# Optimization experiments

Measured on AMD Instinct MI355X. Metric: run time of the kernel, lower is better.

Reference implementation:

```python
import jax, jax.numpy as jnp
import numpy as np

SEMA_DIM = 1024
L1, L2, B = 256, 320, 64


def setup_inputs() -> dict:
    key = jax.random.key(0)
    k1, k2, kw1, kb1, kw2, kb2 = jax.random.split(key, 6)
    D = SEMA_DIM
    s = 1.0 / np.sqrt(D)
    return {
        "r1": jax.random.normal(k1, (L1, B, D), dtype=jnp.float32),
        "r2": jax.random.normal(k2, (L2, B, D), dtype=jnp.float32),
        "W1": jax.random.uniform(kw1, (D, D), jnp.float32, -s, s),
        "b1": jax.random.uniform(kb1, (D,), jnp.float32, -s, s),
        "W2": jax.random.uniform(kw2, (D, D), jnp.float32, -s, s),
        "b2": jax.random.uniform(kb2, (D,), jnp.float32, -s, s),
    }


def _mlp(x, W1, b1, W2, b2):
    # torch Linear: x @ W.T + b
    h = jax.nn.relu(x @ W1.T + b1)
    return h @ W2.T + b2


def reference(r1, r2, W1, b1, W2, b2):
    # (L, B, D) -> mlp -> (B, L, D)
    r1 = jnp.transpose(_mlp(r1, W1, b1, W2, b2), (1, 0, 2))  # [B, L1, D]
    r2 = jnp.transpose(_mlp(r2, W1, b1, W2, b2), (1, 0, 2))  # [B, L2, D]

    o = jnp.einsum("bid,bjd->bij", r1, r2)  # [B, L1, L2]
    o1 = jax.nn.softmax(o, axis=2)           # attend r1 -> r2
    o2 = jax.nn.softmax(o, axis=1)           # attend r2 -> r1

    r1_c = jnp.einsum("bij,bjd->bid", o1, r2)  # [B, L1, D]
    r2_c = jnp.einsum("bij,bid->bjd", o2, r1)  # [B, L2, D]

    r1_pool = jnp.concatenate([r1, r1_c], axis=-1).sum(axis=1) / r1.shape[1]  # [B, 2D]
    r2_pool = jnp.concatenate([r2, r2_c], axis=-1).sum(axis=1) / r2.shape[1]  # [B, 2D]
    return (r1_pool, r2_pool)
```

## Files before the change

kernel.cpp:

```cpp
#include <hip/hip_runtime.h>
#include <stdint.h>

#define L1C 256
#define L2C 320
#define BC  64
#define DC  1024

typedef __bf16 bf16_t;
typedef __bf16 bf16x8 __attribute__((ext_vector_type(8)));
typedef __bf16 bf16x4 __attribute__((ext_vector_type(4)));
typedef float  f32x4  __attribute__((ext_vector_type(4)));

__device__ __forceinline__ void gload16(const void* g, void* l) {
  __builtin_amdgcn_global_load_lds(
      (__attribute__((address_space(1))) void*)g,
      (__attribute__((address_space(3))) void*)l, 16, 0, 0);
}

__global__ __launch_bounds__(256)
void conv_kernel(const float* __restrict__ src, bf16_t* __restrict__ dst, int n4) {
  int i = blockIdx.x * 256 + threadIdx.x;
  const int stride = gridDim.x * 256;
  for (; i < n4; i += stride) {
    float4 v = ((const float4*)src)[i];
    bf16x4 o = { (__bf16)v.x, (__bf16)v.y, (__bf16)v.z, (__bf16)v.w };
    ((bf16x4*)dst)[i] = o;
  }
}

__global__ __launch_bounds__(256)
void w2t_kernel(const float* __restrict__ W2, bf16_t* __restrict__ W2T) {
  __shared__ float tile[32][33];
  const int tx = threadIdx.x & 31, ty = threadIdx.x >> 5;
  const int x0 = blockIdx.x * 32, y0 = blockIdx.y * 32;
#pragma unroll
  for (int k = 0; k < 32; k += 8)
    tile[ty + k][tx] = W2[(size_t)(y0 + ty + k) * 1024 + x0 + tx];
  __syncthreads();
#pragma unroll
  for (int k = 0; k < 32; k += 8)
    W2T[(size_t)(x0 + ty + k) * 1024 + y0 + tx] = (bf16_t)tile[tx][ty + k];
}

__global__ __launch_bounds__(256)
void wb_kernel(const float* __restrict__ W2, const float* __restrict__ b2,
               float* __restrict__ w2b) {
  const int dt = threadIdx.x & 15, kg = threadIdx.x >> 4;
  const int d = blockIdx.x * 16 + dt;
  float s = 0.f;
  for (int k = kg * 64; k < kg * 64 + 64; ++k)
    s += W2[(size_t)k * 1024 + d] * b2[k];
  __shared__ float red[16][17];
  red[kg][dt] = s;
  __syncthreads();
  if (kg == 0) {
    float t = 0.f;
#pragma unroll
    for (int g = 0; g < 16; ++g) t += red[g][dt];
    w2b[d] = t;
  }
}

__global__ __launch_bounds__(512, 2)
void mlp_gemm_f32a(const float* __restrict__ R1, const float* __restrict__ R2,
                   const bf16_t* __restrict__ W, const float* __restrict__ bias,
                   bf16_t* __restrict__ C, int Mtiles,
                   const float* __restrict__ w2b, float* __restrict__ tpart) {
  const int nwg = Mtiles * 4;
  const int cpx = nwg >> 3;
  const int wg  = ((int)blockIdx.x & 7) * cpx + ((int)blockIdx.x >> 3);
  const int mt = wg >> 2, nt = wg & 3;

  __shared__ __align__(16) char lds[147456];

  const int t    = threadIdx.x;
  const int lane = t & 63, wid = t >> 6;
  const int wm = wid >> 2, wn = wid & 3;
  const int rsel = lane & 15, hi = lane >> 4;
  const int t16 = t * 16;

  const int rT = t >> 3;
  const int gT = (t & 7) ^ (rT & 7);
  const float* Abase = (mt < 64) ? (R1 + (size_t)mt * 256 * 1024)
                                 : (R2 + (size_t)(mt - 64) * 256 * 1024);
  const float* pA[4];
#pragma unroll
  for (int l = 0; l < 4; ++l)
    pA[l] = Abase + (size_t)(l * 64 + rT) * 1024 + gT * 4;

  const int P0 = t16, P1 = 8192 + t16;
  const int Lg0 = P0 ^ ((P0 >> 3) & 0x30);
  const int Lg1 = P1 ^ ((P1 >> 3) & 0x30);
  const bf16_t* pB0 = W + (size_t)(nt * 256 + (Lg0 >> 6)) * 1024 + ((Lg0 & 63) >> 1);
  const bf16_t* pB1 = W + (size_t)(nt * 256 + (Lg1 >> 6)) * 1024 + ((Lg1 & 63) >> 1);

  const int rowA = wm * 128 + rsel;
  const int offA0 = (rowA << 7) + (((2 * hi)     ^ (rsel & 7)) << 4);
  const int offA1 = (rowA << 7) + (((2 * hi + 1) ^ (rsel & 7)) << 4);
  const int kchunk = (hi ^ ((rsel >> 1) & 3)) << 4;
  const int offB = 32768 + ((wn * 64 + rsel) << 6) + kchunk;

  f32x4 acc[8][4] = {};
  bf16x8 bfr[4];

#pragma unroll
  for (int p = 0; p < 2; ++p) {
    char* db = lds + p * 49152;
#pragma unroll
    for (int l = 0; l < 4; ++l) gload16(pA[l] + p * 32, db + l * 8192 + t16);
    gload16(pB0 + p * 32, db + 32768 + t16);
    gload16(pB1 + p * 32, db + 40960 + t16);
  }
  asm volatile("s_waitcnt vmcnt(6)" ::: "memory");
  __builtin_amdgcn_s_barrier();
  __builtin_amdgcn_sched_barrier(0);

  int cur = 0;
#pragma unroll 1
  for (int tt = 0; tt < 32; ++tt) {
    const char* rb = lds + cur * 49152;
    int nx = cur + 2; if (nx >= 3) nx -= 3;
    char* sb = lds + nx * 49152;
    const int ks = (tt + 2) * 32;
    bf16x8 af[4];
#pragma unroll
    for (int m = 0; m < 4; ++m) {
      f32x4 a0 = *(const f32x4*)(rb + offA0 + m * 2048);
      f32x4 a1 = *(const f32x4*)(rb + offA1 + m * 2048);
      af[m] = bf16x8{ (bf16_t)a0[0], (bf16_t)a0[1], (bf16_t)a0[2], (bf16_t)a0[3],
                      (bf16_t)a1[0], (bf16_t)a1[1], (bf16_t)a1[2], (bf16_t)a1[3] };
    }
#pragma unroll
    for (int n = 0; n < 4; ++n) bfr[n] = *(const bf16x8*)(rb + offB + n * 1024);
    if (tt < 30) {
#pragma unroll
      for (int l = 0; l < 4; ++l) gload16(pA[l] + ks, sb + l * 8192 + t16);
    }
    __builtin_amdgcn_s_setprio(1);
#pragma unroll
    for (int m = 0; m < 4; ++m)
#pragma unroll
      for (int n = 0; n < 4; ++n)
        acc[m][n] = __builtin_amdgcn_mfma_f32_16x16x32_bf16(af[m], bfr[n], acc[m][n], 0, 0, 0);
    __builtin_amdgcn_s_setprio(0);
    __builtin_amdgcn_s_barrier();
    __builtin_amdgcn_sched_barrier(0);
#pragma unroll
    for (int m = 0; m < 4; ++m) {
      f32x4 a0 = *(const f32x4*)(rb + offA0 + (m + 4) * 2048);
      f32x4 a1 = *(const f32x4*)(rb + offA1 + (m + 4) * 2048);
      af[m] = bf16x8{ (bf16_t)a0[0], (bf16_t)a0[1], (bf16_t)a0[2], (bf16_t)a0[3],
                      (bf16_t)a1[0], (bf16_t)a1[1], (bf16_t)a1[2], (bf16_t)a1[3] };
    }
    if (tt < 30) {
      gload16(pB0 + ks, sb + 32768 + t16);
      gload16(pB1 + ks, sb + 40960 + t16);
    }
    __builtin_amdgcn_s_setprio(1);
#pragma unroll
    for (int m = 0; m < 4; ++m)
#pragma unroll
      for (int n = 0; n < 4; ++n)
        acc[m + 4][n] = __builtin_amdgcn_mfma_f32_16x16x32_bf16(af[m], bfr[n], acc[m + 4][n], 0, 0, 0);
    __builtin_amdgcn_s_setprio(0);
    if (tt < 30)       asm volatile("s_waitcnt vmcnt(6)" ::: "memory");
    else if (tt == 30) asm volatile("s_waitcnt vmcnt(0)" ::: "memory");
    __builtin_amdgcn_s_barrier();
    __builtin_amdgcn_sched_barrier(0);
    cur = (cur + 1 == 3) ? 0 : cur + 1;
  }

  const int row0 = mt * 256 + wm * 128 + hi * 4;
  const int col0 = nt * 256 + wn * 64 + rsel;
  float bv[4];
#pragma unroll
  for (int n = 0; n < 4; ++n) bv[n] = bias[col0 + n * 16];
#pragma unroll
  for (int m = 0; m < 8; ++m) {
#pragma unroll
    for (int q = 0; q < 4; ++q) {
      const size_t rr = (size_t)(row0 + m * 16 + q) * 1024;
#pragma unroll
      for (int n = 0; n < 4; ++n) {
        float v = fmaxf(acc[m][n][q] + bv[n], 0.f);
        C[rr + col0 + n * 16] = (bf16_t)v;
      }
    }
  }

  {
    float wv[4];
#pragma unroll
    for (int n = 0; n < 4; ++n) wv[n] = w2b[col0 + n * 16];
    float* tp = tpart + (size_t)(nt * 4 + wn) * 36864;
#pragma unroll
    for (int m = 0; m < 8; ++m) {
#pragma unroll
      for (int q = 0; q < 4; ++q) {
        float s = 0.f;
#pragma unroll
        for (int n = 0; n < 4; ++n) {
          float v = fmaxf(acc[m][n][q] + bv[n], 0.f);
          v = (float)(bf16_t)v;
          s += v * wv[n];
        }
        s += __shfl_xor(s, 1);
        s += __shfl_xor(s, 2);
        s += __shfl_xor(s, 4);
        s += __shfl_xor(s, 8);
        if (rsel == 0)
          tp[row0 + m * 16 + q] = s;
      }
    }
  }
}

__global__ __launch_bounds__(256)
void t_red(const float* __restrict__ tp, float* __restrict__ tT1,
           float* __restrict__ tT2) {
  const int r = blockIdx.x * 256 + threadIdx.x;
  float s = 0.f;
#pragma unroll
  for (int k = 0; k < 16; ++k) s += tp[(size_t)k * 36864 + r];
  if (r < 16384) tT1[(r & 63) * L1C + (r >> 6)] = s;
  else {
    const int r2 = r - 16384;
    tT2[(r2 & 63) * L2C + (r2 >> 6)] = s;
  }
}

__global__ __launch_bounds__(512, 2)
void mlp_gemm8(const bf16_t* __restrict__ A, const bf16_t* __restrict__ W,
               const float* __restrict__ bias, bf16_t* __restrict__ C,
               int Mtiles, int relu) {
  const int nwg = Mtiles * 4;
  const int cpx = nwg >> 3;
  const int wg  = ((int)blockIdx.x & 7) * cpx + ((int)blockIdx.x >> 3);
  const int mt = wg >> 2, nt = wg & 3;

  __shared__ __align__(16) char lds[131072];

  const int t    = threadIdx.x;
  const int lane = t & 63, wid = t >> 6;
  const int wm = wid >> 2, wn = wid & 3;
  const int rsel = lane & 15, hi = lane >> 4;
  const int t16 = t * 16;

  const int P0 = t16, P1 = 8192 + t16;
  const int Lg0 = P0 ^ ((P0 >> 3) & 0x30);
  const int Lg1 = P1 ^ ((P1 >> 3) & 0x30);
  const int rS0 = Lg0 >> 6, cS0 = (Lg0 & 63) >> 1;
  const int rS1 = Lg1 >> 6, cS1 = (Lg1 & 63) >> 1;
  const bf16_t* pA0 = A + (size_t)(mt * 256 + rS0) * 1024 + cS0;
  const bf16_t* pA1 = A + (size_t)(mt * 256 + rS1) * 1024 + cS1;
  const bf16_t* pB0 = W + (size_t)(nt * 256 + rS0) * 1024 + cS0;
  const bf16_t* pB1 = W + (size_t)(nt * 256 + rS1) * 1024 + cS1;

  const int kchunk = (hi ^ ((rsel >> 1) & 3)) << 4;
  const int offA = ((wm * 128 + rsel) << 6) + kchunk;
  const int offB = 16384 + ((wn * 64 + rsel) << 6) + kchunk;

  f32x4 acc[8][4] = {};
  bf16x8 bfr[4];

#pragma unroll
  for (int p = 0; p < 3; ++p) {
    char* db = lds + p * 32768;
    gload16(pA0 + p * 32, db + t16);
    gload16(pA1 + p * 32, db + 8192 + t16);
    gload16(pB0 + p * 32, db + 16384 + t16);
    gload16(pB1 + p * 32, db + 24576 + t16);
  }
  asm volatile("s_waitcnt vmcnt(8)" ::: "memory");
  __builtin_amdgcn_s_barrier();
  __builtin_amdgcn_sched_barrier(0);

#pragma unroll 1
  for (int tt = 0; tt < 32; ++tt) {
    const char* rb = lds + (tt & 3) * 32768;
    char* sb = lds + ((tt + 3) & 3) * 32768;
    const int ks = (tt + 3) * 32;
    bf16x8 af[4];
#pragma unroll
    for (int m = 0; m < 4; ++m) af[m] = *(const bf16x8*)(rb + offA + m * 1024);
#pragma unroll
    for (int n = 0; n < 4; ++n) bfr[n] = *(const bf16x8*)(rb + offB + n * 1024);
    if (tt < 29) {
      gload16(pA0 + ks, sb + t16);
      gload16(pA1 + ks, sb + 8192 + t16);
    }
    __builtin_amdgcn_s_setprio(1);
#pragma unroll
    for (int m = 0; m < 4; ++m)
#pragma unroll
      for (int n = 0; n < 4; ++n)
        acc[m][n] = __builtin_amdgcn_mfma_f32_16x16x32_bf16(af[m], bfr[n], acc[m][n], 0, 0, 0);
    __builtin_amdgcn_s_setprio(0);
    __builtin_amdgcn_s_barrier();
    __builtin_amdgcn_sched_barrier(0);
#pragma unroll
    for (int m = 0; m < 4; ++m) af[m] = *(const bf16x8*)(rb + offA + (m + 4) * 1024);
    if (tt < 29) {
      gload16(pB0 + ks, sb + 16384 + t16);
      gload16(pB1 + ks, sb + 24576 + t16);
    }
    __builtin_amdgcn_s_setprio(1);
#pragma unroll
    for (int m = 0; m < 4; ++m)
#pragma unroll
      for (int n = 0; n < 4; ++n)
        acc[m + 4][n] = __builtin_amdgcn_mfma_f32_16x16x32_bf16(af[m], bfr[n], acc[m + 4][n], 0, 0, 0);
    __builtin_amdgcn_s_setprio(0);
    if (tt < 29)       asm volatile("s_waitcnt vmcnt(8)" ::: "memory");
    else if (tt == 29) asm volatile("s_waitcnt vmcnt(4)" ::: "memory");
    else if (tt == 30) asm volatile("s_waitcnt vmcnt(0)" ::: "memory");
    __builtin_amdgcn_s_barrier();
    __builtin_amdgcn_sched_barrier(0);
  }

  const int row0 = mt * 256 + wm * 128 + hi * 4;
  const int col0 = nt * 256 + wn * 64 + rsel;
  float bv[4];
#pragma unroll
  for (int n = 0; n < 4; ++n) bv[n] = bias[col0 + n * 16];
#pragma unroll
  for (int m = 0; m < 8; ++m) {
#pragma unroll
    for (int q = 0; q < 4; ++q) {
      const size_t rr = (size_t)(row0 + m * 16 + q) * 1024;
#pragma unroll
      for (int n = 0; n < 4; ++n) {
        float v = acc[m][n][q] + bv[n];
        if (relu) v = fmaxf(v, 0.f);
        C[rr + col0 + n * 16] = (bf16_t)v;
      }
    }
  }
}

__global__ __launch_bounds__(256)
void gemmK(const bf16_t* __restrict__ A, const bf16_t* __restrict__ W,
           float* __restrict__ P, int KS) {
  const int slice = (int)blockIdx.x >> 6;
  const int tl = (int)blockIdx.x & 63;
  const int mt = tl >> 3, nt = tl & 7;
  const int koff = slice * KS;

  const int f = threadIdx.x;
  const int lane = f & 63, w = f >> 6;
  const int sRow = f >> 2, sCol8 = (f & 3) * 8;

  const bf16_t* Ab = A + (size_t)mt * 128 * 1024 + (size_t)sRow * 1024 + sCol8;
  const bf16_t* Bb = W + (size_t)nt * 128 * 1024 + (size_t)sRow * 1024 + sCol8;

  __shared__ __align__(16) bf16_t sA[128 * 32];
  __shared__ __align__(16) bf16_t sB[128 * 32];
  bf16_t* sAp = sA + sRow * 32 + sCol8;
  bf16_t* sBp = sB + sRow * 32 + sCol8;

  const int wr = (w >> 1) * 64, wc = (w & 1) * 64;
  const int rsel = lane & 15, koff2 = (lane >> 4) * 8;
  const bf16_t* rA = sA + (wr + rsel) * 32 + koff2;
  const bf16_t* rB = sB + (wc + rsel) * 32 + koff2;

  f32x4 acc[4][4] = {};
  for (int kt = koff; kt < koff + KS; kt += 32) {
    __syncthreads();
    gload16(Ab + kt,             sAp);
    gload16(Ab + kt + 64 * 1024, sAp + 64 * 32);
    gload16(Bb + kt,             sBp);
    gload16(Bb + kt + 64 * 1024, sBp + 64 * 32);
    asm volatile("s_waitcnt vmcnt(0)" ::: "memory");
    __syncthreads();
    bf16x8 af[4], bfv[4];
#pragma unroll
    for (int m = 0; m < 4; ++m) af[m] = *(const bf16x8*)(rA + m * 16 * 32);
#pragma unroll
    for (int n = 0; n < 4; ++n) bfv[n] = *(const bf16x8*)(rB + n * 16 * 32);
#pragma unroll
    for (int m = 0; m < 4; ++m)
#pragma unroll
      for (int n = 0; n < 4; ++n)
        acc[m][n] = __builtin_amdgcn_mfma_f32_16x16x32_bf16(af[m], bfv[n], acc[m][n], 0, 0, 0);
  }

  float* Pb = P + (size_t)slice * 1048576;
  const int row0 = mt * 128 + wr + (lane >> 4) * 4;
  const int col0 = nt * 128 + wc + rsel;
#pragma unroll
  for (int n = 0; n < 4; ++n) {
    const int c = col0 + n * 16;
#pragma unroll
    for (int m = 0; m < 4; ++m) {
      const int r = row0 + m * 16;
#pragma unroll
      for (int q = 0; q < 4; ++q)
        Pb[(size_t)(r + q) * 1024 + c] = acc[m][n][q];
    }
  }
}

__global__ __launch_bounds__(256)
void g_reduce(const float* __restrict__ Gp, bf16_t* __restrict__ GB) {
  const int i4 = blockIdx.x * 256 + threadIdx.x;
  float4 a = ((const float4*)Gp)[i4];
  float4 b = ((const float4*)(Gp + 1048576))[i4];
  float4 c = ((const float4*)(Gp + 2097152))[i4];
  float4 d = ((const float4*)(Gp + 3145728))[i4];
  bf16x4 o = { (bf16_t)(a.x + b.x + c.x + d.x), (bf16_t)(a.y + b.y + c.y + d.y),
               (bf16_t)(a.z + b.z + c.z + d.z), (bf16_t)(a.w + b.w + c.w + d.w) };
  ((bf16x4*)GB)[i4] = o;
}

__global__ __launch_bounds__(256)
void pool_gemmK(const bf16_t* __restrict__ A, const bf16_t* __restrict__ W,
                float* __restrict__ P) {
  const int slice = (int)blockIdx.x >> 4;
  const int tl = (int)blockIdx.x & 15;
  const int mt = tl >> 3, nt = tl & 7;
  const int koff = slice * 128;

  const int f = threadIdx.x;
  const int lane = f & 63, w = f >> 6;
  const int sRow = f >> 2, sCol8 = (f & 3) * 8;

  const bf16_t* Ab = A + (size_t)mt * 128 * 1024 + (size_t)sRow * 1024 + sCol8;
  const bf16_t* Bb = W + (size_t)nt * 128 * 1024 + (size_t)sRow * 1024 + sCol8;

  __shared__ __align__(16) bf16_t sA[128 * 32];
  __shared__ __align__(16) bf16_t sB[128 * 32];
  bf16_t* sAp = sA + sRow * 32 + sCol8;
  bf16_t* sBp = sB + sRow * 32 + sCol8;

  const int wr = (w >> 1) * 64, wc = (w & 1) * 64;
  const int rsel = lane & 15, koff2 = (lane >> 4) * 8;
  const bf16_t* rA = sA + (wr + rsel) * 32 + koff2;
  const bf16_t* rB = sB + (wc + rsel) * 32 + koff2;

  f32x4 acc[4][4] = {};
  for (int kt = koff; kt < koff + 128; kt += 32) {
    __syncthreads();
    gload16(Ab + kt,             sAp);
    gload16(Ab + kt + 64 * 1024, sAp + 64 * 32);
    gload16(Bb + kt,             sBp);
    gload16(Bb + kt + 64 * 1024, sBp + 64 * 32);
    asm volatile("s_waitcnt vmcnt(0)" ::: "memory");
    __syncthreads();
    bf16x8 af[4], bfv[4];
#pragma unroll
    for (int m = 0; m < 4; ++m) af[m] = *(const bf16x8*)(rA + m * 16 * 32);
#pragma unroll
    for (int n = 0; n < 4; ++n) bfv[n] = *(const bf16x8*)(rB + n * 16 * 32);
#pragma unroll
    for (int m = 0; m < 4; ++m)
#pragma unroll
      for (int n = 0; n < 4; ++n)
        acc[m][n] = __builtin_amdgcn_mfma_f32_16x16x32_bf16(af[m], bfv[n], acc[m][n], 0, 0, 0);
  }

  float* Pb = P + (size_t)slice * 262144;
  const int row0 = mt * 128 + wr + (lane >> 4) * 4;
  const int col0 = nt * 128 + wc + rsel;
#pragma unroll
  for (int n = 0; n < 4; ++n) {
    const int c = col0 + n * 16;
#pragma unroll
    for (int m = 0; m < 4; ++m) {
      const int r = row0 + m * 16;
#pragma unroll
      for (int q = 0; q < 4; ++q)
        Pb[(size_t)(r + q) * 1024 + c] = acc[m][n][q];
    }
  }
}

__global__ __launch_bounds__(256)
void pool_reduce(const float* __restrict__ Pp, const float* __restrict__ b2,
                 float* __restrict__ out) {
  const int idx = blockIdx.x * 256 + threadIdx.x;
  const int r = idx >> 10, c = idx & 1023;
  float s = b2[c];
#pragma unroll
  for (int sl = 0; sl < 8; ++sl) s += Pp[(size_t)sl * 262144 + idx];
  const int g = r >> 6, b = r & 63;
  out[(size_t)(g >> 1) * 131072 + (size_t)b * 2048 + (g & 1) * 1024 + c] = s;
}

__global__ __launch_bounds__(256)
void logits_gemm(const bf16_t* __restrict__ Y1, const bf16_t* __restrict__ Y2,
                 float* __restrict__ O) {
  const int wg = ((int)blockIdx.x & 7) * 48 + ((int)blockIdx.x >> 3);
  const int b = wg / 6, t6 = wg % 6;
  const int mt = t6 / 3, nt = t6 % 3;

  __shared__ __align__(16) char lds[65536];

  const int t = threadIdx.x;
  const int lane = t & 63, w = t >> 6;
  const int sRow = t >> 2;
  const int sCol8 = (((t & 3) ^ ((t >> 3) & 3))) * 8;
  const int t16 = t * 16;

  const int i0 = mt * 128 + sRow;
  const int i1 = i0 + 64;
  int j0 = nt * 128 + sRow;      if (j0 > L2C - 1) j0 = L2C - 1;
  int j1 = nt * 128 + sRow + 64; if (j1 > L2C - 1) j1 = L2C - 1;
  const bf16_t* A0 = Y1 + ((size_t)i0 * BC + b) * DC + sCol8;
  const bf16_t* A1 = Y1 + ((size_t)i1 * BC + b) * DC + sCol8;
  const bf16_t* B0 = Y2 + ((size_t)j0 * BC + b) * DC + sCol8;
  const bf16_t* B1 = Y2 + ((size_t)j1 * BC + b) * DC + sCol8;

  const int wr = (w >> 1) * 64, wc = (w & 1) * 64;
  const int rsel = lane & 15, hi = lane >> 4;
  const int kchunk = (hi ^ ((rsel >> 1) & 3)) << 4;
  const int offA = ((wr + rsel) << 6) + kchunk;
  const int offB = 8192 + ((wc + rsel) << 6) + kchunk;

  f32x4 acc[4][4] = {};

#pragma unroll
  for (int p = 0; p < 3; ++p) {
    char* db = lds + p * 16384;
    gload16(A0 + p * 32, db + t16);
    gload16(A1 + p * 32, db + 4096 + t16);
    gload16(B0 + p * 32, db + 8192 + t16);
    gload16(B1 + p * 32, db + 12288 + t16);
  }
  asm volatile("s_waitcnt vmcnt(8)" ::: "memory");
  __builtin_amdgcn_s_barrier();
  __builtin_amdgcn_sched_barrier(0);

#pragma unroll 1
  for (int tt = 0; tt < 32; ++tt) {
    const char* rb = lds + (tt & 3) * 16384;
    char* sb = lds + ((tt + 3) & 3) * 16384;
    const int ks = (tt + 3) * 32;
    bf16x8 af[4], bfv[4];
#pragma unroll
    for (int m = 0; m < 4; ++m) af[m] = *(const bf16x8*)(rb + offA + m * 1024);
#pragma unroll
    for (int n = 0; n < 4; ++n) bfv[n] = *(const bf16x8*)(rb + offB + n * 1024);
    if (tt < 29) {
      gload16(A0 + ks, sb + t16);
      gload16(A1 + ks, sb + 4096 + t16);
      gload16(B0 + ks, sb + 8192 + t16);
      gload16(B1 + ks, sb + 12288 + t16);
    }
    __builtin_amdgcn_s_setprio(1);
#pragma unroll
    for (int m = 0; m < 4; ++m)
#pragma unroll
      for (int n = 0; n < 4; ++n)
        acc[m][n] = __builtin_amdgcn_mfma_f32_16x16x32_bf16(af[m], bfv[n], acc[m][n], 0, 0, 0);
    __builtin_amdgcn_s_setprio(0);
    if (tt < 29)       asm volatile("s_waitcnt vmcnt(8)" ::: "memory");
    else if (tt == 29) asm volatile("s_waitcnt vmcnt(4)" ::: "memory");
    else if (tt == 30) asm volatile("s_waitcnt vmcnt(0)" ::: "memory");
    __builtin_amdgcn_s_barrier();
    __builtin_amdgcn_sched_barrier(0);
  }

  float* Ob = O + (size_t)b * L1C * L2C;
  const int row0 = mt * 128 + wr + hi * 4;
  const int col0 = nt * 128 + wc + rsel;
#pragma unroll
  for (int n = 0; n < 4; ++n) {
    const int c = col0 + n * 16;
    if (c < L2C) {
#pragma unroll
      for (int m = 0; m < 4; ++m) {
        const int r = row0 + m * 16;
#pragma unroll
        for (int q = 0; q < 4; ++q)
          Ob[(size_t)(r + q) * L2C + c] = acc[m][n][q];
      }
    }
  }
}

__global__ __launch_bounds__(256)
void row_stats(const float* __restrict__ O, const float* __restrict__ tT2,
               float* __restrict__ rowM, float* __restrict__ rowInv) {
  const int gw = blockIdx.x * 4 + (threadIdx.x >> 6);
  const int lane = threadIdx.x & 63;
  const int b = gw >> 8;
  const float* row = O + (size_t)gw * L2C;
  const float* t2 = tT2 + b * L2C;
  float v[5];
  float m = -1e30f;
#pragma unroll
  for (int t = 0; t < 5; ++t) { v[t] = row[t * 64 + lane] + t2[t * 64 + lane]; m = fmaxf(m, v[t]); }
#pragma unroll
  for (int off = 32; off; off >>= 1) m = fmaxf(m, __shfl_xor(m, off));
  float s = 0.f;
#pragma unroll
  for (int t = 0; t < 5; ++t) s += __expf(v[t] - m);
#pragma unroll
  for (int off = 32; off; off >>= 1) s += __shfl_xor(s, off);
  if (lane == 0) { rowM[gw] = m; rowInv[gw] = 1.f / s; }
}

__global__ __launch_bounds__(256)
void col_stats_c1(const float* __restrict__ O, const float* __restrict__ tT1,
                  const float* __restrict__ tT2,
                  const float* __restrict__ rowM, const float* __restrict__ rowInv,
                  float* __restrict__ colM, float* __restrict__ colInv,
                  float* __restrict__ c1) {
  const int b = blockIdx.x / 5, jb = blockIdx.x % 5;
  const int jl = threadIdx.x & 63, ig = threadIdx.x >> 6;
  const int j = jb * 64 + jl;
  const float* Ob = O + (size_t)b * L1C * L2C + j;
  const float* rM = rowM + b * L1C;
  const float* rI = rowInv + b * L1C;
  const float* t1 = tT1 + b * L1C;
  const float t2j = tT2[b * L2C + j];
  float m = -1e30f, s = 0.f, cp = 0.f;
  for (int i = ig; i < L1C; i += 4) {
    float ov = Ob[(size_t)i * L2C];
    float v = ov + t1[i];
    float mn = fmaxf(m, v);
    s = s * __expf(m - mn) + __expf(v - mn);
    m = mn;
    cp += __expf(ov + t2j - rM[i]) * rI[i];
  }
  __shared__ float sm[4][64], ss[4][64], sc[4][64];
  sm[ig][jl] = m; ss[ig][jl] = s; sc[ig][jl] = cp;
  __syncthreads();
  if (ig == 0) {
    for (int g = 1; g < 4; ++g) {
      float mg = sm[g][jl], sg = ss[g][jl];
      float mn = fmaxf(m, mg);
      s = s * __expf(m - mn) + sg * __expf(mg - mn);
      m = mn;
      cp += sc[g][jl];
    }
    colM[b * L2C + j] = m;
    colInv[b * L2C + j] = 1.f / s;
    c1[b * L2C + j] = cp;
  }
}

__global__ __launch_bounds__(256)
void c2_kernel(const float* __restrict__ O, const float* __restrict__ tT1,
               const float* __restrict__ colM, const float* __restrict__ colInv,
               float* __restrict__ c2) {
  const int gw = blockIdx.x * 4 + (threadIdx.x >> 6);
  const int lane = threadIdx.x & 63;
  const int b = gw >> 8;
  const float* row = O + (size_t)gw * L2C;
  const float* cM = colM + b * L2C;
  const float* cI = colInv + b * L2C;
  const float t1i = tT1[b * L1C + (gw & 255)];
  float s = 0.f;
#pragma unroll
  for (int t = 0; t < 5; ++t) {
    const int j = t * 64 + lane;
    s += __expf(row[j] + t1i - cM[j]) * cI[j];
  }
#pragma unroll
  for (int off = 32; off; off >>= 1) s += __shfl_xor(s, off);
  if (lane == 0) c2[gw] = s;
}

__global__ __launch_bounds__(256)
void u_kernel(const bf16_t* __restrict__ H, const float* __restrict__ c1,
              const float* __restrict__ c2, bf16_t* __restrict__ Ub) {
  const int b = blockIdx.x >> 2;
  const int d = (blockIdx.x & 3) * 256 + threadIdx.x;
  const bf16_t* H2 = H + (size_t)L1C * BC * DC;
  float s1 = 0.f, s1c = 0.f, s2 = 0.f, s2c = 0.f;
  const float* c2b = c2 + b * L1C;
  for (int i = 0; i < L1C; ++i) {
    float v = (float)H[((size_t)i * BC + b) * DC + d];
    s1 += v; s1c += c2b[i] * v;
  }
  const float* c1b = c1 + b * L2C;
  for (int j = 0; j < L2C; ++j) {
    float v = (float)H2[((size_t)j * BC + b) * DC + d];
    s2 += v; s2c += c1b[j] * v;
  }
  Ub[(size_t)(0 * 64 + b) * 1024 + d] = (bf16_t)(s1  * (1.f / L1C));
  Ub[(size_t)(1 * 64 + b) * 1024 + d] = (bf16_t)(s2c * (1.f / L1C));
  Ub[(size_t)(2 * 64 + b) * 1024 + d] = (bf16_t)(s2  * (1.f / L2C));
  Ub[(size_t)(3 * 64 + b) * 1024 + d] = (bf16_t)(s1c * (1.f / L2C));
}

extern "C" void kernel_launch(void* const* d_in, const int* in_sizes, int n_in,
                              void* d_out, int out_size, void* d_ws, size_t ws_size,
                              hipStream_t stream) {
  const float* r1 = (const float*)d_in[0];
  const float* r2 = (const float*)d_in[1];
  const float* W1 = (const float*)d_in[2];
  const float* b1 = (const float*)d_in[3];
  const float* W2 = (const float*)d_in[4];
  const float* b2 = (const float*)d_in[5];
  float* out = (float*)d_out;
  char* ws = (char*)d_ws;

  const size_t M1 = (size_t)L1C * BC;
  const size_t M2 = (size_t)L2C * BC;
  const size_t Mt = M1 + M2;

  size_t off = 0;
  bf16_t* XB  = (bf16_t*)(ws + off); off += Mt * DC * 2;
  bf16_t* HB  = (bf16_t*)(ws + off); off += Mt * DC * 2;
  bf16_t* WB1 = (bf16_t*)(ws + off); off += (size_t)DC * DC * 2;
  bf16_t* WB2 = (bf16_t*)(ws + off); off += (size_t)DC * DC * 2;
  bf16_t* W2T = (bf16_t*)(ws + off); off += (size_t)DC * DC * 2;
  bf16_t* GB  = (bf16_t*)(ws + off); off += (size_t)DC * DC * 2;
  float* w2b   = (float*)(ws + off); off += 4096;
  float* zb    = (float*)(ws + off); off += 4096;
  float* tT1   = (float*)(ws + off); off += BC * L1C * 4;
  float* tT2   = (float*)(ws + off); off += BC * L2C * 4;
  float* rowM  = (float*)(ws + off); off += BC * L1C * 4;
  float* rowIv = (float*)(ws + off); off += BC * L1C * 4;
  float* colM  = (float*)(ws + off); off += BC * L2C * 4;
  float* colIv = (float*)(ws + off); off += BC * L2C * 4;
  float* c1v   = (float*)(ws + off); off += BC * L2C * 4;
  float* c2v   = (float*)(ws + off); off += BC * L1C * 4;
  bf16_t* Ub   = (bf16_t*)(ws + off); off += 256 * DC * 2;
  float* tpart = (float*)(ws + off); off += (size_t)16 * Mt * 4;

  bf16_t* Z = XB;
  float*  O = (float*)((char*)XB + 35651584);
  float*  Gpart = (float*)((char*)XB + 58720256);
  float*  Ppart = (float*)HB;
  bf16_t* H2 = HB + M1 * DC;

  conv_kernel<<<512, 256, 0, stream>>>(W1, WB1, (int)((size_t)DC * DC / 4));
  conv_kernel<<<512, 256, 0, stream>>>(W2, WB2, (int)((size_t)DC * DC / 4));
  w2t_kernel<<<dim3(32, 32), 256, 0, stream>>>(W2, W2T);
  wb_kernel<<<64, 256, 0, stream>>>(W2, b2, w2b);
  (void)hipMemsetAsync(zb, 0, 4096, stream);

  mlp_gemm_f32a<<<576, 512, 0, stream>>>(r1, r2, WB1, b1, HB, 144, w2b, tpart);
  t_red<<<144, 256, 0, stream>>>(tpart, tT1, tT2);

  gemmK<<<256, 256, 0, stream>>>(W2T, W2T, Gpart, 256);
  g_reduce<<<1024, 256, 0, stream>>>(Gpart, GB);

  mlp_gemm8<<<256, 512, 0, stream>>>(HB, GB, zb, Z, 64, 0);

  logits_gemm<<<384, 256, 0, stream>>>(Z, H2, O);

  row_stats<<<4096, 256, 0, stream>>>(O, tT2, rowM, rowIv);
  col_stats_c1<<<320, 256, 0, stream>>>(O, tT1, tT2, rowM, rowIv, colM, colIv, c1v);
  c2_kernel<<<4096, 256, 0, stream>>>(O, tT1, colM, colIv, c2v);

  u_kernel<<<256, 256, 0, stream>>>(HB, c1v, c2v, Ub);
  pool_gemmK<<<128, 256, 0, stream>>>(Ub, WB2, Ppart);
  pool_reduce<<<1024, 256, 0, stream>>>(Ppart, b2, out);
}
```

Baseline: 304.0 us.

## Pre-convert activations to bf16 and use 128x128 first-layer GEMM with separate t reduction

Replaces the fused first-layer GEMM, which loaded fp32 activations into LDS and converted them per tile, with two steps. A separate conversion pass now writes bf16 copies of r1/r2, and a smaller 128x128-tile, 256-thread GEMM runs with a 4-stage LDS pipeline. The fused t-vector epilogue is replaced by a standalone kernel that re-reads H and dots each row with w2b. This trades extra global traffic (conversion pass, re-reading H) for higher occupancy, cheaper LDS fragment loads and no in-loop conversion.

```diff
diff --git a/kernel.cpp b/kernel.cpp
--- a/kernel.cpp
+++ b/kernel.cpp
@@ -61,122 +61,82 @@
   }
 }
 
-__global__ __launch_bounds__(512, 2)
-void mlp_gemm_f32a(const float* __restrict__ R1, const float* __restrict__ R2,
-                   const bf16_t* __restrict__ W, const float* __restrict__ bias,
-                   bf16_t* __restrict__ C, int Mtiles,
-                   const float* __restrict__ w2b, float* __restrict__ tpart) {
-  const int nwg = Mtiles * 4;
-  const int cpx = nwg >> 3;
-  const int wg  = ((int)blockIdx.x & 7) * cpx + ((int)blockIdx.x >> 3);
-  const int mt = wg >> 2, nt = wg & 3;
-
-  __shared__ __align__(16) char lds[147456];
-
-  const int t    = threadIdx.x;
-  const int lane = t & 63, wid = t >> 6;
-  const int wm = wid >> 2, wn = wid & 3;
+__global__ __launch_bounds__(256)
+void gemm1_128(const bf16_t* __restrict__ A, const bf16_t* __restrict__ W,
+               const float* __restrict__ bias, bf16_t* __restrict__ C) {
+  const int wg = ((int)blockIdx.x & 7) * 288 + ((int)blockIdx.x >> 3);
+  const int mt = wg >> 3, nt = wg & 7;
+
+  __shared__ __align__(16) char lds[65536];
+
+  const int t = threadIdx.x;
+  const int lane = t & 63, w = t >> 6;
+  const int sRow = t >> 2;
+  const int sCol8 = (((t & 3) ^ ((t >> 3) & 3))) * 8;
+  const int t16 = t * 16;
+
+  const bf16_t* A0 = A + (size_t)(mt * 128 + sRow) * 1024 + sCol8;
+  const bf16_t* A1 = A0 + (size_t)64 * 1024;
+  const bf16_t* B0 = W + (size_t)(nt * 128 + sRow) * 1024 + sCol8;
+  const bf16_t* B1 = B0 + (size_t)64 * 1024;
+
+  const int wr = (w >> 1) * 64, wc = (w & 1) * 64;
   const int rsel = lane & 15, hi = lane >> 4;
-  const int t16 = t * 16;
-
-  const int rT = t >> 3;
-  const int gT = (t & 7) ^ (rT & 7);
-  const float* Abase = (mt < 64) ? (R1 + (size_t)mt * 256 * 1024)
-                                 : (R2 + (size_t)(mt - 64) * 256 * 1024);
-  const float* pA[4];
-#pragma unroll
-  for (int l = 0; l < 4; ++l)
-    pA[l] = Abase + (size_t)(l * 64 + rT) * 1024 + gT * 4;
-
-  const int P0 = t16, P1 = 8192 + t16;
-  const int Lg0 = P0 ^ ((P0 >> 3) & 0x30);
-  const int Lg1 = P1 ^ ((P1 >> 3) & 0x30);
-  const bf16_t* pB0 = W + (size_t)(nt * 256 + (Lg0 >> 6)) * 1024 + ((Lg0 & 63) >> 1);
-  const bf16_t* pB1 = W + (size_t)(nt * 256 + (Lg1 >> 6)) * 1024 + ((Lg1 & 63) >> 1);
-
-  const int rowA = wm * 128 + rsel;
-  const int offA0 = (rowA << 7) + (((2 * hi)     ^ (rsel & 7)) << 4);
-  const int offA1 = (rowA << 7) + (((2 * hi + 1) ^ (rsel & 7)) << 4);
   const int kchunk = (hi ^ ((rsel >> 1) & 3)) << 4;
-  const int offB = 32768 + ((wn * 64 + rsel) << 6) + kchunk;
-
-  f32x4 acc[8][4] = {};
-  bf16x8 bfr[4];
-
-#pragma unroll
-  for (int p = 0; p < 2; ++p) {
-    char* db = lds + p * 49152;
-#pragma unroll
-    for (int l = 0; l < 4; ++l) gload16(pA[l] + p * 32, db + l * 8192 + t16);
-    gload16(pB0 + p * 32, db + 32768 + t16);
-    gload16(pB1 + p * 32, db + 40960 + t16);
-  }
-  asm volatile("s_waitcnt vmcnt(6)" ::: "memory");
+  const int offA = ((wr + rsel) << 6) + kchunk;
+  const int offB = 8192 + ((wc + rsel) << 6) + kchunk;
+
+  f32x4 acc[4][4] = {};
+
+#pragma unroll
+  for (int p = 0; p < 3; ++p) {
+    char* db = lds + p * 16384;
+    gload16(A0 + p * 32, db + t16);
+    gload16(A1 + p * 32, db + 4096 + t16);
+    gload16(B0 + p * 32, db + 8192 + t16);
+    gload16(B1 + p * 32, db + 12288 + t16);
+  }
+  asm volatile("s_waitcnt vmcnt(8)" ::: "memory");
   __builtin_amdgcn_s_barrier();
   __builtin_amdgcn_sched_barrier(0);
 
-  int cur = 0;
 #pragma unroll 1
   for (int tt = 0; tt < 32; ++tt) {
-    const char* rb = lds + cur * 49152;
-    int nx = cur + 2; if (nx >= 3) nx -= 3;
-    char* sb = lds + nx * 49152;
-    const int ks = (tt + 2) * 32;
-    bf16x8 af[4];
-#pragma unroll
-    for (int m = 0; m < 4; ++m) {
-      f32x4 a0 = *(const f32x4*)(rb + offA0 + m * 2048);
-      f32x4 a1 = *(const f32x4*)(rb + offA1 + m * 2048);
-      af[m] = bf16x8{ (bf16_t)a0[0], (bf16_t)a0[1], (bf16_t)a0[2], (bf16_t)a0[3],
-                      (bf16_t)a1[0], (bf16_t)a1[1], (bf16_t)a1[2], (bf16_t)a1[3] };
-    }
-#pragma unroll
-    for (int n = 0; n < 4; ++n) bfr[n] = *(const bf16x8*)(rb + offB + n * 1024);
-    if (tt < 30) {
-#pragma unroll
-      for (int l = 0; l < 4; ++l) gload16(pA[l] + ks, sb + l * 8192 + t16);
+    const char* rb = lds + (tt & 3) * 16384;
+    char* sb = lds + ((tt + 3) & 3) * 16384;
+    const int ks = (tt + 3) * 32;
+    bf16x8 af[4], bfv[4];
+#pragma unroll
+    for (int m = 0; m < 4; ++m) af[m] = *(const bf16x8*)(rb + offA + m * 1024);
+#pragma unroll
+    for (int n = 0; n < 4; ++n) bfv[n] = *(const bf16x8*)(rb + offB + n * 1024);
+    if (tt < 29) {
+      gload16(A0 + ks, sb + t16);
+      gload16(A1 + ks, sb + 4096 + t16);
+      gload16(B0 + ks, sb + 8192 + t16);
+      gload16(B1 + ks, sb + 12288 + t16);
     }
     __builtin_amdgcn_s_setprio(1);
 #pragma unroll
     for (int m = 0; m < 4; ++m)
 #pragma unroll
       for (int n = 0; n < 4; ++n)
-        acc[m][n] = __builtin_amdgcn_mfma_f32_16x16x32_bf16(af[m], bfr[n], acc[m][n], 0, 0, 0);
+        acc[m][n] = __builtin_amdgcn_mfma_f32_16x16x32_bf16(af[m], bfv[n], acc[m][n], 0, 0, 0);
     __builtin_amdgcn_s_setprio(0);
-    __builtin_amdgcn_s_barrier();
-    __builtin_amdgcn_sched_barrier(0);
-#pragma unroll
-    for (int m = 0; m < 4; ++m) {
-      f32x4 a0 = *(const f32x4*)(rb + offA0 + (m + 4) * 2048);
-      f32x4 a1 = *(const f32x4*)(rb + offA1 + (m + 4) * 2048);
-      af[m] = bf16x8{ (bf16_t)a0[0], (bf16_t)a0[1], (bf16_t)a0[2], (bf16_t)a0[3],
-                      (bf16_t)a1[0], (bf16_t)a1[1], (bf16_t)a1[2], (bf16_t)a1[3] };
-    }
-    if (tt < 30) {
-      gload16(pB0 + ks, sb + 32768 + t16);
-      gload16(pB1 + ks, sb + 40960 + t16);
-    }
-    __builtin_amdgcn_s_setprio(1);
-#pragma unroll
-    for (int m = 0; m < 4; ++m)
-#pragma unroll
-      for (int n = 0; n < 4; ++n)
-        acc[m + 4][n] = __builtin_amdgcn_mfma_f32_16x16x32_bf16(af[m], bfr[n], acc[m + 4][n], 0, 0, 0);
-    __builtin_amdgcn_s_setprio(0);
-    if (tt < 30)       asm volatile("s_waitcnt vmcnt(6)" ::: "memory");
+    if (tt < 29)       asm volatile("s_waitcnt vmcnt(8)" ::: "memory");
+    else if (tt == 29) asm volatile("s_waitcnt vmcnt(4)" ::: "memory");
     else if (tt == 30) asm volatile("s_waitcnt vmcnt(0)" ::: "memory");
     __builtin_amdgcn_s_barrier();
     __builtin_amdgcn_sched_barrier(0);
-    cur = (cur + 1 == 3) ? 0 : cur + 1;
-  }
-
-  const int row0 = mt * 256 + wm * 128 + hi * 4;
-  const int col0 = nt * 256 + wn * 64 + rsel;
+  }
+
+  const int row0 = mt * 128 + wr + hi * 4;
+  const int col0 = nt * 128 + wc + rsel;
   float bv[4];
 #pragma unroll
   for (int n = 0; n < 4; ++n) bv[n] = bias[col0 + n * 16];
 #pragma unroll
-  for (int m = 0; m < 8; ++m) {
+  for (int m = 0; m < 4; ++m) {
 #pragma unroll
     for (int q = 0; q < 4; ++q) {
       const size_t rr = (size_t)(row0 + m * 16 + q) * 1024;
@@ -187,45 +147,27 @@
       }
     }
   }
-
-  {
-    float wv[4];
-#pragma unroll
-    for (int n = 0; n < 4; ++n) wv[n] = w2b[col0 + n * 16];
-    float* tp = tpart + (size_t)(nt * 4 + wn) * 36864;
-#pragma unroll
-    for (int m = 0; m < 8; ++m) {
-#pragma unroll
-      for (int q = 0; q < 4; ++q) {
-        float s = 0.f;
-#pragma unroll
-        for (int n = 0; n < 4; ++n) {
-          float v = fmaxf(acc[m][n][q] + bv[n], 0.f);
-          v = (float)(bf16_t)v;
-          s += v * wv[n];
-        }
-        s += __shfl_xor(s, 1);
-        s += __shfl_xor(s, 2);
-        s += __shfl_xor(s, 4);
-        s += __shfl_xor(s, 8);
-        if (rsel == 0)
-          tp[row0 + m * 16 + q] = s;
-      }
-    }
-  }
-}
-
-__global__ __launch_bounds__(256)
-void t_red(const float* __restrict__ tp, float* __restrict__ tT1,
-           float* __restrict__ tT2) {
-  const int r = blockIdx.x * 256 + threadIdx.x;
+}
+
+__global__ __launch_bounds__(256)
+void t_kernel(const bf16_t* __restrict__ H, const float* __restrict__ w2b,
+              float* __restrict__ tT1, float* __restrict__ tT2) {
+  const int wv = threadIdx.x >> 6, lane = threadIdx.x & 63;
+  const int r = blockIdx.x * 4 + wv;
+  const bf16_t* hrow = H + (size_t)r * 1024;
   float s = 0.f;
 #pragma unroll
-  for (int k = 0; k < 16; ++k) s += tp[(size_t)k * 36864 + r];
-  if (r < 16384) tT1[(r & 63) * L1C + (r >> 6)] = s;
-  else {
-    const int r2 = r - 16384;
-    tT2[(r2 & 63) * L2C + (r2 >> 6)] = s;
+  for (int h = 0; h < 2; ++h) {
+    bf16x8 v = *(const bf16x8*)(hrow + h * 512 + lane * 8);
+#pragma unroll
+    for (int e = 0; e < 8; ++e) s += (float)v[e] * w2b[h * 512 + lane * 8 + e];
+  }
+#pragma unroll
+  for (int off = 32; off; off >>= 1) s += __shfl_xor(s, off);
+  if (lane == 0) {
+    const int b = r & 63;
+    if (r < 16384) tT1[b * L1C + (r >> 6)] = s;
+    else           tT2[b * L2C + ((r - 16384) >> 6)] = s;
   }
 }
 
@@ -719,7 +661,6 @@
   float* c1v   = (float*)(ws + off); off += BC * L2C * 4;
   float* c2v   = (float*)(ws + off); off += BC * L1C * 4;
   bf16_t* Ub   = (bf16_t*)(ws + off); off += 256 * DC * 2;
-  float* tpart = (float*)(ws + off); off += (size_t)16 * Mt * 4;
 
   bf16_t* Z = XB;
   float*  O = (float*)((char*)XB + 35651584);
@@ -727,14 +668,16 @@
   float*  Ppart = (float*)HB;
   bf16_t* H2 = HB + M1 * DC;
 
-  conv_kernel<<<512, 256, 0, stream>>>(W1, WB1, (int)((size_t)DC * DC / 4));
-  conv_kernel<<<512, 256, 0, stream>>>(W2, WB2, (int)((size_t)DC * DC / 4));
+  conv_kernel<<<2048, 256, 0, stream>>>(r1, XB,           (int)(M1 * DC / 4));
+  conv_kernel<<<2048, 256, 0, stream>>>(r2, XB + M1 * DC, (int)(M2 * DC / 4));
+  conv_kernel<<<512,  256, 0, stream>>>(W1, WB1, (int)((size_t)DC * DC / 4));
+  conv_kernel<<<512,  256, 0, stream>>>(W2, WB2, (int)((size_t)DC * DC / 4));
   w2t_kernel<<<dim3(32, 32), 256, 0, stream>>>(W2, W2T);
   wb_kernel<<<64, 256, 0, stream>>>(W2, b2, w2b);
   (void)hipMemsetAsync(zb, 0, 4096, stream);
 
-  mlp_gemm_f32a<<<576, 512, 0, stream>>>(r1, r2, WB1, b1, HB, 144, w2b, tpart);
-  t_red<<<144, 256, 0, stream>>>(tpart, tT1, tT2);
+  gemm1_128<<<2304, 256, 0, stream>>>(XB, WB1, b1, HB);
+  t_kernel<<<9216, 256, 0, stream>>>(HB, w2b, tT1, tT2);
 
   gemmK<<<256, 256, 0, stream>>>(W2T, W2T, Gpart, 256);
   g_reduce<<<1024, 256, 0, stream>>>(Gpart, GB);
```

New measurement: 299.9 us. No clear change (-1.4%).
